# Kernel tuning notes

Hardware: AMD Instinct MI355X
Metric: run time of the kernel (lower is better)

The kernel has to match this reference:

```python
import jax, jax.numpy as jnp
import numpy as np

Z_DIM = 3
H = 128
N_BLOCKS = 4
N = 30000
E = 180000
T = 2


def _mlp2(x, W1, b1, W2, b2):
    return jnp.maximum(x @ W1 + b1, 0.0) @ W2 + b2


def _stats(x, eps=1e-8):
    # batch mean/std as accumulated by the running-stat Normalizer (buffers -> no grad)
    m = x.mean(0)
    v = jnp.maximum((x * x).mean(0) - m * m, 0.0)
    s = jnp.maximum(jnp.sqrt(v), eps)
    return jax.lax.stop_gradient(m), jax.lax.stop_gradient(s)


def setup_inputs() -> dict:
    key = jax.random.key(0)
    ks = jax.random.split(key, 32)

    def w(k, shape, fan_in):
        return jax.random.normal(k, shape, jnp.float32) / np.sqrt(fan_in).astype(np.float32)

    inp = {}
    inp["z"] = jax.random.normal(ks[0], (T, N, Z_DIM), jnp.float32)
    inp["z_target"] = jax.random.normal(ks[1], (N, Z_DIM), jnp.float32)
    inp["pos"] = jax.random.uniform(ks[2], (N, 2), jnp.float32)
    # encoder node MLP: z_dim -> H -> H
    inp["enc_node_W1"] = w(ks[3], (Z_DIM, H), Z_DIM)
    inp["enc_node_b1"] = jnp.zeros((H,), jnp.float32)
    inp["enc_node_W2"] = w(ks[4], (H, H), H)
    inp["enc_node_b2"] = jnp.zeros((H,), jnp.float32)
    # encoder edge MLP: edge_dim(3) -> H -> H
    inp["enc_edge_W1"] = w(ks[5], (3, H), 3)
    inp["enc_edge_b1"] = jnp.zeros((H,), jnp.float32)
    inp["enc_edge_W2"] = w(ks[6], (H, H), H)
    inp["enc_edge_b2"] = jnp.zeros((H,), jnp.float32)
    # decoder MLP: H -> H -> z_dim
    inp["dec_W1"] = w(ks[7], (H, H), H)
    inp["dec_b1"] = jnp.zeros((H,), jnp.float32)
    inp["dec_W2"] = w(ks[8], (H, Z_DIM), H)
    inp["dec_b2"] = jnp.zeros((Z_DIM,), jnp.float32)
    # GraphNetBlocks, stacked over n_blocks
    inp["blk_edge_W1"] = w(ks[9], (N_BLOCKS, 3 * H, H), 3 * H)
    inp["blk_edge_b1"] = jnp.zeros((N_BLOCKS, H), jnp.float32)
    inp["blk_edge_W2"] = w(ks[10], (N_BLOCKS, H, H), H)
    inp["blk_edge_b2"] = jnp.zeros((N_BLOCKS, H), jnp.float32)
    inp["blk_node_W1"] = w(ks[11], (N_BLOCKS, 2 * H, H), 2 * H)
    inp["blk_node_b1"] = jnp.zeros((N_BLOCKS, H), jnp.float32)
    inp["blk_node_W2"] = w(ks[12], (N_BLOCKS, H, H), H)
    inp["blk_node_b2"] = jnp.zeros((N_BLOCKS, H), jnp.float32)
    # bidirectional mesh edges (triangles_to_edges output)
    inp["senders"] = jax.random.randint(ks[13], (E,), 0, N, jnp.int64)
    inp["receivers"] = jax.random.randint(ks[14], (E,), 0, N, jnp.int64)
    return inp


def reference(z, z_target, pos,
              enc_node_W1, enc_node_b1, enc_node_W2, enc_node_b2,
              enc_edge_W1, enc_edge_b1, enc_edge_W2, enc_edge_b2,
              dec_W1, dec_b1, dec_W2, dec_b2,
              blk_edge_W1, blk_edge_b1, blk_edge_W2, blk_edge_b2,
              blk_node_W1, blk_node_b1, blk_node_W2, blk_node_b2,
              senders, receivers):
    zl = z[-1]                                   # [N, z_dim]
    n_nodes = zl.shape[0]

    # --- build_graph ---
    rel = pos[senders] - pos[receivers]          # [E, 2]
    ef_raw = jnp.concatenate([rel, jnp.linalg.norm(rel, axis=1, keepdims=True)], axis=1)  # [E, 3]
    em, es = _stats(ef_raw)
    ef = _mlp2((ef_raw - em) / es, enc_edge_W1, enc_edge_b1, enc_edge_W2, enc_edge_b2)    # [E, H]
    nm, ns = _stats(zl)
    nf = _mlp2((zl - nm) / ns, enc_node_W1, enc_node_b1, enc_node_W2, enc_node_b2)        # [N, H]

    # --- message passing blocks ---
    def block(carry, p):
        nf, ef = carry
        eW1, eb1, eW2, eb2, nW1, nb1, nW2, nb2 = p
        e_in = jnp.concatenate([ef, nf[senders], nf[receivers]], axis=1)   # [E, 3H]
        ef = _mlp2(e_in, eW1, eb1, eW2, eb2) + ef
        agg = jax.ops.segment_sum(ef, receivers, num_segments=n_nodes)    # [N, H]
        n_in = jnp.concatenate([nf, agg], axis=1)                          # [N, 2H]
        nf = _mlp2(n_in, nW1, nb1, nW2, nb2) + nf
        return (nf, ef), None

    (nf, ef), _ = jax.lax.scan(block, (nf, ef),
                               (blk_edge_W1, blk_edge_b1, blk_edge_W2, blk_edge_b2,
                                blk_node_W1, blk_node_b1, blk_node_W2, blk_node_b2))

    # --- decode + loss ---
    output = _mlp2(nf, dec_W1, dec_b1, dec_W2, dec_b2)                     # [N, z_dim]
    target = z_target - zl
    om, os = _stats(target)
    target_normalized = (target - om) / os
    loss = jnp.mean((target_normalized - output) ** 2)

    z_update = jax.lax.stop_gradient(output) * os + om                     # Normalizer.inverse(detach)
    z_pred = zl + z_update
    rmse = jnp.mean(jnp.sqrt(jnp.mean((z_pred - z_target) ** 2, axis=0)))
    return z_pred, loss, rmse
```

## Files before the change

kernel.cpp:

```cpp
#include <hip/hip_runtime.h>
#include <hip/hip_bf16.h>
#include <math.h>

#define HDIM 128
#define TPB 256

typedef __attribute__((ext_vector_type(8))) short bf16x8;
typedef __attribute__((ext_vector_type(4))) float f32x4;

static inline int ceil_div(int a, int b){ return (a + b - 1) / b; }

__device__ __forceinline__ float wave_sum(float v){
#pragma unroll
  for (int o = 32; o > 0; o >>= 1) v += __shfl_down(v, o, 64);
  return v;
}
__device__ __forceinline__ int wave_sum_i(int v){
#pragma unroll
  for (int o = 32; o > 0; o >>= 1) v += __shfl_down(v, o, 64);
  return v;
}

__device__ __forceinline__ short f2bf(float f){
  __hip_bfloat16 h = __float2bfloat16(f);
  return *reinterpret_cast<short*>(&h);
}
__device__ __forceinline__ float bfb2f(short s){
  unsigned int u = ((unsigned int)(unsigned short)s) << 16;
  return __builtin_bit_cast(float, u);
}

__device__ __forceinline__ void gl_lds16(const short* g, short* l){
  __builtin_amdgcn_global_load_lds(
      (const __attribute__((address_space(1))) void*)g,
      (__attribute__((address_space(3))) void*)l, 16, 0, 0);
}

__global__ void prep_a(const int* __restrict__ rcv, int* __restrict__ deg, int E, int neb,
                       const float* __restrict__ zl, const float* __restrict__ zt,
                       float* __restrict__ npart, int N, int nnb,
                       const float* __restrict__ encEW2,
                       const float* __restrict__ encNW2,
                       const float* __restrict__ decW1,
                       const float* __restrict__ beW1,
                       const float* __restrict__ beW2,
                       const float* __restrict__ bnW1,
                       const float* __restrict__ bnW2,
                       __hip_bfloat16* __restrict__ wp){
  __shared__ float red[4][12];
  const int bx = blockIdx.x, tid = threadIdx.x;
  if (bx < neb){
    int e = bx * 256 + tid;
    if (e < E) atomicAdd(&deg[rcv[e]], 1);
    return;
  }
  if (bx < neb + nnb){
    int b = bx - neb;
    int w = tid >> 6, l = tid & 63;
    int n = b * 256 + tid;
    float s[12];
#pragma unroll
    for (int i = 0; i < 12; i++) s[i] = 0.f;
    if (n < N){
#pragma unroll
      for (int d = 0; d < 3; d++){
        float z = zl[3*n+d];
        float t = zt[3*n+d] - z;
        s[d]   = z;  s[3+d] = z*z;
        s[6+d] = t;  s[9+d] = t*t;
      }
    }
#pragma unroll
    for (int i = 0; i < 12; i++) s[i] = wave_sum(s[i]);
    if (l == 0)
#pragma unroll
      for (int i = 0; i < 12; i++) red[w][i] = s[i];
    __syncthreads();
    if (tid < 12)
      npart[(size_t)b * 12 + tid] =
        red[0][tid] + red[1][tid] + red[2][tid] + red[3][tid];
    return;
  }
  int pid = bx - neb - nnb;
  int y = pid / 192;
  int x = pid - y * 192;
  const float* src; __hip_bfloat16* dst; int K;
  if (y == 0){ src = encEW2; dst = wp;          K = 128; }
  else if (y == 1){ src = encNW2; dst = wp + 16384; K = 128; }
  else if (y == 2){ src = decW1;  dst = wp + 32768; K = 128; }
  else {
    int b = (y - 3) >> 2, j = (y - 3) & 3;
    __hip_bfloat16* base = wp + 49152 + b * 114688;
    if (j == 0){ src = beW1 + b*49152; dst = base;          K = 384; }
    else if (j == 1){ src = beW2 + b*16384; dst = base + 49152; K = 128; }
    else if (j == 2){ src = bnW1 + b*32768; dst = base + 65536; K = 256; }
    else { src = bnW2 + b*16384; dst = base + 98304; K = 128; }
  }
  int id = x * 256 + tid;
  if (id >= 128 * K) return;
  int c = id >> 12;
  int r = id & 4095;
  int t = r >> 9;
  int l = (r >> 3) & 63;
  int j = r & 7;
  int k = c * 32 + ((l >> 4) << 3) + j;
  int n = t * 16 + (l & 15);
  dst[id] = __float2bfloat16(src[k * 128 + n]);
}

__global__ void scan_pass1(const int* __restrict__ deg, int* __restrict__ bsum, int N){
  __shared__ int red[4];
  int tid = threadIdx.x;
  int base = blockIdx.x * 1024;
  int s = 0;
  for (int i = tid; i < 1024; i += 256){
    int idx = base + i;
    if (idx < N) s += deg[idx];
  }
  s = wave_sum_i(s);
  if ((tid & 63) == 0) red[tid >> 6] = s;
  __syncthreads();
  if (tid == 0) bsum[blockIdx.x] = red[0] + red[1] + red[2] + red[3];
}

__global__ void scan_pass3(const int* __restrict__ deg, const int* __restrict__ bsum,
                           int nsb, int* __restrict__ cursor, int N){
  __shared__ int tsum[256];
  __shared__ int base_s;
  int tid = threadIdx.x;
  if (tid == 0){
    int acc = 0;
    for (int b = 0; b < (int)blockIdx.x; b++) acc += bsum[b];
    base_s = acc;
  }
  int base = blockIdx.x * 1024;
  int i0 = base + tid * 4;
  int v[4];
  int s = 0;
#pragma unroll
  for (int k = 0; k < 4; k++){
    int idx = i0 + k;
    v[k] = (idx < N) ? deg[idx] : 0;
    s += v[k];
  }
  tsum[tid] = s;
  __syncthreads();
  for (int off = 1; off < 256; off <<= 1){
    int val = (tid >= off) ? tsum[tid - off] : 0;
    __syncthreads();
    tsum[tid] += val;
    __syncthreads();
  }
  int excl = (tid == 0) ? 0 : tsum[tid - 1];
  int b = base_s + excl;
#pragma unroll
  for (int k = 0; k < 4; k++){
    int idx = i0 + k;
    if (idx < N){
      cursor[idx] = b;
      b += v[k];
    }
  }
}

__global__ void edge_prep(const float* __restrict__ pos,
                          const int* __restrict__ snd,
                          const int* __restrict__ rcv,
                          int* __restrict__ cursor,
                          int* __restrict__ psnd,
                          int* __restrict__ prcv,
                          float* __restrict__ ef_raw,
                          float* __restrict__ epart, int E){
  __shared__ float red[4][6];
  int tid = threadIdx.x, w = tid >> 6, l = tid & 63;
  int e = blockIdx.x * blockDim.x + tid;
  float s[6] = {0.f,0.f,0.f,0.f,0.f,0.f};
  if (e < E){
    int si = snd[e], ri = rcv[e];
    int p = atomicAdd(&cursor[ri], 1);
    psnd[p] = si;
    prcv[p] = ri;
    float rx = pos[2*si]   - pos[2*ri];
    float ry = pos[2*si+1] - pos[2*ri+1];
    float nm = sqrtf(rx*rx + ry*ry);
    ef_raw[3*p]   = rx;
    ef_raw[3*p+1] = ry;
    ef_raw[3*p+2] = nm;
    s[0] = rx; s[1] = ry; s[2] = nm;
    s[3] = rx*rx; s[4] = ry*ry; s[5] = nm*nm;
  }
#pragma unroll
  for (int k = 0; k < 6; k++) s[k] = wave_sum(s[k]);
  if (l == 0)
#pragma unroll
    for (int k = 0; k < 6; k++) red[w][k] = s[k];
  __syncthreads();
  if (tid < 6)
    epart[(size_t)blockIdx.x * 6 + tid] =
      red[0][tid] + red[1][tid] + red[2][tid] + red[3][tid];
}

__global__ void reduce_finalize(const float* __restrict__ ep, int ne,
                                const float* __restrict__ np_, int nn,
                                float* __restrict__ fin, int E, int N){
  __shared__ float red[4];
  __shared__ float raw[18];
  int tid = threadIdx.x, w = tid >> 6, l = tid & 63;
  for (int j = 0; j < 6; j++){
    float s = 0.f;
    for (int b = tid; b < ne; b += 256) s += ep[(size_t)b * 6 + j];
    s = wave_sum(s);
    if (l == 0) red[w] = s;
    __syncthreads();
    if (tid == 0) raw[j] = red[0] + red[1] + red[2] + red[3];
    __syncthreads();
  }
  for (int j = 0; j < 12; j++){
    float s = 0.f;
    for (int b = tid; b < nn; b += 256) s += np_[(size_t)b * 12 + j];
    s = wave_sum(s);
    if (l == 0) red[w] = s;
    __syncthreads();
    if (tid == 0) raw[6 + j] = red[0] + red[1] + red[2] + red[3];
    __syncthreads();
  }
  if (tid == 0){
#pragma unroll
    for (int d = 0; d < 3; d++){
      float cE = (float)E, cN = (float)N;
      float m, v;
      m = raw[0+d] / cE; v = fmaxf(raw[3+d]/cE - m*m, 0.f);
      fin[0+d] = m;  fin[3+d]  = fmaxf(sqrtf(v), 1e-8f);
      m = raw[6+d] / cN; v = fmaxf(raw[9+d]/cN - m*m, 0.f);
      fin[6+d] = m;  fin[9+d]  = fmaxf(sqrtf(v), 1e-8f);
      m = raw[12+d] / cN; v = fmaxf(raw[15+d]/cN - m*m, 0.f);
      fin[12+d] = m; fin[15+d] = fmaxf(sqrtf(v), 1e-8f);
    }
  }
}

__launch_bounds__(256)
__global__ void encoder_both(const float* __restrict__ eraw,
                             const float* __restrict__ zl,
                             const float* __restrict__ fin,
                             const float* __restrict__ eW1, const float* __restrict__ eb1,
                             const float* __restrict__ nW1, const float* __restrict__ nb1,
                             const __hip_bfloat16* __restrict__ wp,
                             const float* __restrict__ eb2, const float* __restrict__ nb2,
                             __hip_bfloat16* __restrict__ efo, __hip_bfloat16* __restrict__ nfo,
                             int E, int N, int EB){
  __shared__ __align__(16) short bsh[16384];
  const int tid = threadIdx.x, w = tid >> 6, l = tid & 63, m = l & 15, q = l >> 4;
  const bool ise = ((int)blockIdx.x < EB);
  const float* raw = ise ? eraw : zl;
  const float* mptr = fin + (ise ? 0 : 6);
  const float* sptr = fin + (ise ? 3 : 9);
  const float* W1 = ise ? eW1 : nW1;
  const float* b1 = ise ? eb1 : nb1;
  const float* b2 = ise ? eb2 : nb2;
  const short* wsrc = (const short*)wp + (ise ? 0 : 16384);
  __hip_bfloat16* out = ise ? efo : nfo;
  const int rows = ise ? E : N;
  const int bx = ise ? (int)blockIdx.x : (int)blockIdx.x - EB;
#pragma unroll
  for (int i = 0; i < 8; i++){
    int inst = w * 8 + i;
    gl_lds16(wsrc + inst * 512 + l * 8, &bsh[inst * 512]);
  }
  float s0 = mptr[0], s1 = mptr[1], s2 = mptr[2];
  float d0 = sptr[0], d1 = sptr[1], d2 = sptr[2];
  const int row0 = bx * 64 + w * 16;
  const int ra = min(row0 + m, rows - 1);
  float x0 = (raw[3*ra]   - s0) / d0;
  float x1 = (raw[3*ra+1] - s1) / d1;
  float x2 = (raw[3*ra+2] - s2) / d2;
  bf16x8 afr[4];
#pragma unroll
  for (int c = 0; c < 4; c++){
    int nb = c * 32 + q * 8;
#pragma unroll
    for (int j = 0; j < 8; j++){
      float h = b1[nb+j] + x0 * W1[nb+j] + x1 * W1[128+nb+j] + x2 * W1[256+nb+j];
      afr[c][j] = f2bf(fmaxf(h, 0.f));
    }
  }
  f32x4 acc[8];
#pragma unroll
  for (int t = 0; t < 8; t++) acc[t] = (f32x4){0.f,0.f,0.f,0.f};
  __syncthreads();
#pragma unroll
  for (int c = 0; c < 4; c++){
#pragma unroll
    for (int t = 0; t < 8; t++){
      bf16x8 b = *(const bf16x8*)&bsh[(c*8 + t)*512 + l*8];
      acc[t] = __builtin_amdgcn_mfma_f32_16x16x32_bf16(afr[c], b, acc[t], 0, 0, 0);
    }
  }
  const int row_d = row0 + q * 4;
#pragma unroll
  for (int t = 0; t < 8; t++){
    int col = t * 16 + m;
    float bb = b2[col];
#pragma unroll
    for (int r = 0; r < 4; r++){
      int e = row_d + r;
      if (e < rows) out[(size_t)e * HDIM + col] = __float2bfloat16(acc[t][r] + bb);
    }
  }
}

__launch_bounds__(256)
__global__ void msg_pre(const __hip_bfloat16* __restrict__ nf,
                        const __hip_bfloat16* __restrict__ eWf,
                        __hip_bfloat16* __restrict__ u,
                        float* __restrict__ agg, int N){
  __shared__ __align__(16) short wsh[16384];
  const int tid = threadIdx.x, w = tid >> 6, l = tid & 63, m = l & 15, q = l >> 4;
  const short* wsrc = (const short*)eWf + 4 * 4096;
#pragma unroll
  for (int i = 0; i < 8; i++){
    int f = w * 8 + i;
    gl_lds16(wsrc + f * 512 + l * 8, &wsh[f * 512]);
  }
  {
    float* az = agg + (size_t)blockIdx.x * 8192;
#pragma unroll
    for (int i = 0; i < 8; i++)
      *(f32x4*)(az + (size_t)(i * 256 + tid) * 4) = (f32x4){0.f,0.f,0.f,0.f};
  }
  const int row0 = blockIdx.x * 64 + w * 16;
  const int ra = min(row0 + m, N - 1);
  const short* pa = (const short*)nf + (size_t)ra * HDIM + q * 8;
  bf16x8 afr[4];
#pragma unroll
  for (int c = 0; c < 4; c++) afr[c] = *(const bf16x8*)(pa + c * 32);
  f32x4 acc[8];
#pragma unroll
  for (int t = 0; t < 8; t++) acc[t] = (f32x4){0.f,0.f,0.f,0.f};
  __syncthreads();
#pragma unroll
  for (int c = 0; c < 4; c++)
#pragma unroll
    for (int t = 0; t < 8; t++){
      bf16x8 b = *(const bf16x8*)&wsh[(c*8 + t)*512 + l*8];
      acc[t] = __builtin_amdgcn_mfma_f32_16x16x32_bf16(afr[c], b, acc[t], 0, 0, 0);
    }
  const int row_d = row0 + q * 4;
#pragma unroll
  for (int t = 0; t < 8; t++){
    int col = t * 16 + m;
#pragma unroll
    for (int r = 0; r < 4; r++){
      int n = row_d + r;
      if (n < N) u[(size_t)n * 256 + col] = __float2bfloat16(acc[t][r]);
    }
  }
  __syncthreads();
#pragma unroll
  for (int i = 0; i < 8; i++){
    int f = w * 8 + i;
    gl_lds16(wsrc + 16384 + f * 512 + l * 8, &wsh[f * 512]);
  }
#pragma unroll
  for (int t = 0; t < 8; t++) acc[t] = (f32x4){0.f,0.f,0.f,0.f};
  __syncthreads();
#pragma unroll
  for (int c = 0; c < 4; c++)
#pragma unroll
    for (int t = 0; t < 8; t++){
      bf16x8 b = *(const bf16x8*)&wsh[(c*8 + t)*512 + l*8];
      acc[t] = __builtin_amdgcn_mfma_f32_16x16x32_bf16(afr[c], b, acc[t], 0, 0, 0);
    }
#pragma unroll
  for (int t = 0; t < 8; t++){
    int col = 128 + t * 16 + m;
#pragma unroll
    for (int r = 0; r < 4; r++){
      int n = row_d + r;
      if (n < N) u[(size_t)n * 256 + col] = __float2bfloat16(acc[t][r]);
    }
  }
}

__launch_bounds__(512)
__global__ void edge_block(const int* __restrict__ psnd,
                           const int* __restrict__ prcv,
                           const __hip_bfloat16* __restrict__ u,
                           __hip_bfloat16* __restrict__ ef,
                           const __hip_bfloat16* __restrict__ Wfrag,
                           const float* __restrict__ b1,
                           const float* __restrict__ b2,
                           float* __restrict__ agg,
                           int do_write, int E){
  __shared__ __align__(16) short bsh[16384];
  __shared__ __align__(16) short hsh[8][16][136];
  __shared__ int rsh[128];
  const int tid = threadIdx.x, w = tid >> 6, l = tid & 63, m = l & 15, q = l >> 4;
  const short* wsrc = (const short*)Wfrag;
  const int row0 = blockIdx.x * 128 + w * 16;
  const int grow = min(row0 + (l >> 2), E - 1);
  const int us_row = psnd[grow], ur_row = prcv[grow];
  if ((l & 3) == 0) rsh[w * 16 + (l >> 2)] = ur_row;
#pragma unroll
  for (int i = 0; i < 4; i++){
    int inst = i * 8 + w;
    gl_lds16(wsrc + inst * 512 + l * 8, &bsh[inst * 512]);
  }
  const int ra = min(row0 + m, E - 1);
  const short* pe = (const short*)ef + (size_t)ra * HDIM + q * 8;
  bf16x8 afr[4];
#pragma unroll
  for (int c = 0; c < 4; c++) afr[c] = *(const bf16x8*)(pe + c * 32);
  {
    const short* pus = (const short*)u + (size_t)us_row * 256 + (l & 3) * 32;
    const short* pur = (const short*)u + (size_t)ur_row * 256 + 128 + (l & 3) * 32;
    short* hdst = &hsh[w][l >> 2][(l & 3) * 32];
#pragma unroll
    for (int k = 0; k < 4; k++){
      bf16x8 a = *(const bf16x8*)(pus + k * 8);
      bf16x8 b = *(const bf16x8*)(pur + k * 8);
      bf16x8 s;
#pragma unroll
      for (int j = 0; j < 8; j++) s[j] = f2bf(bfb2f(a[j]) + bfb2f(b[j]));
      *(bf16x8*)(hdst + k * 8) = s;
    }
  }
  f32x4 acc[8];
#pragma unroll
  for (int t = 0; t < 8; t++) acc[t] = (f32x4){0.f,0.f,0.f,0.f};
  __syncthreads();
#pragma unroll
  for (int c = 0; c < 4; c++){
#pragma unroll
    for (int t = 0; t < 8; t++){
      bf16x8 b = *(const bf16x8*)&bsh[(c*8 + t)*512 + l*8];
      acc[t] = __builtin_amdgcn_mfma_f32_16x16x32_bf16(afr[c], b, acc[t], 0, 0, 0);
    }
  }
  __syncthreads();
#pragma unroll
  for (int i = 0; i < 4; i++){
    int inst = i * 8 + w;
    gl_lds16(wsrc + 49152 + inst * 512 + l * 8, &bsh[inst * 512]);
  }
#pragma unroll
  for (int t = 0; t < 8; t++){
    float bb = b1[t * 16 + m];
#pragma unroll
    for (int r = 0; r < 4; r++){
      float uval = bfb2f(hsh[w][q*4 + r][t*16 + m]);
      hsh[w][q*4 + r][t*16 + m] = f2bf(fmaxf(acc[t][r] + uval + bb, 0.f));
    }
  }
  __syncthreads();
  bf16x8 ah[4];
  const short* ph = &hsh[w][m][0] + q * 8;
#pragma unroll
  for (int c = 0; c < 4; c++) ah[c] = *(const bf16x8*)(ph + c * 32);
#pragma unroll
  for (int t = 0; t < 8; t++) acc[t] = (f32x4){0.f,0.f,0.f,0.f};
#pragma unroll
  for (int c = 0; c < 4; c++){
#pragma unroll
    for (int t = 0; t < 8; t++){
      bf16x8 b = *(const bf16x8*)&bsh[(c*8 + t)*512 + l*8];
      acc[t] = __builtin_amdgcn_mfma_f32_16x16x32_bf16(ah[c], b, acc[t], 0, 0, 0);
    }
  }
#pragma unroll
  for (int t = 0; t < 8; t++){
    float bb = b2[t * 16 + m];
#pragma unroll
    for (int r = 0; r < 4; r++)
      hsh[w][q*4 + r][t*16 + m] = f2bf(acc[t][r] + bb);
  }
  const int orow = row0 + (l >> 2);
  const int orc = min(orow, E - 1);
  const short* pold = (const short*)ef + (size_t)orc * HDIM + (l & 3) * 32;
  short* hslot = &hsh[w][l >> 2][(l & 3) * 32];
  short* dst = (short*)ef + (size_t)orc * HDIM + (l & 3) * 32;
  const bool wr = (orow < E) && do_write;
#pragma unroll
  for (int k = 0; k < 4; k++){
    bf16x8 vnew = *(const bf16x8*)(hslot + k * 8);
    bf16x8 vo   = *(const bf16x8*)(pold + k * 8);
    bf16x8 vr;
#pragma unroll
    for (int j = 0; j < 8; j++) vr[j] = f2bf(bfb2f(vnew[j]) + bfb2f(vo[j]));
    *(bf16x8*)(hslot + k * 8) = vr;
    if (wr) *(bf16x8*)(dst + k * 8) = vr;
  }
  __syncthreads();
  {
    const int c = tid & 127;
    const int g = tid >> 7;
    const int nval = min(128, E - (int)blockIdx.x * 128);
    const int e0 = g * 32;
    if (e0 < nval){
      const int e1 = min(e0 + 32, nval);
      float run = 0.f; int cur = -1; int runstart = e0;
#pragma unroll
      for (int half = 0; half < 2; half++){
        float v[16]; int rv[16];
#pragma unroll
        for (int k = 0; k < 16; k++){
          int e = e0 + half * 16 + k;
          v[k]  = bfb2f(hsh[(e >> 4) & 7][e & 15][c]);
          rv[k] = rsh[e & 127];
        }
#pragma unroll
        for (int k = 0; k < 16; k++){
          int e = e0 + half * 16 + k;
          if (e < e1){
            if (rv[k] != cur){
              if (cur >= 0){
                if (runstart == e0) atomicAdd(&agg[(size_t)cur * 128 + c], run);
                else                agg[(size_t)cur * 128 + c] = run;
              }
              cur = rv[k]; run = 0.f; runstart = e;
            }
            run += v[k];
          }
        }
      }
      atomicAdd(&agg[(size_t)cur * 128 + c], run);
    }
  }
}

#define NB_COMPUTE_CHUNK(c) do {                                               \
  const short* bb_ = &bsh[(((c) >> 1) & 1) * 8192 + ((c) & 1) * 4096];         \
  _Pragma("unroll")                                                            \
  for (int t = 0; t < 8; t++){                                                 \
    bf16x8 b = *(const bf16x8*)(bb_ + t * 512 + l * 8);                        \
    acc[t] = __builtin_amdgcn_mfma_f32_16x16x32_bf16(afr[c], b, acc[t], 0, 0, 0); \
  }                                                                            \
} while(0)

__launch_bounds__(256)
__global__ void node_block(const float* __restrict__ agg,
                           __hip_bfloat16* __restrict__ nf,
                           const __hip_bfloat16* __restrict__ Wfrag,
                           const float* __restrict__ b1,
                           const float* __restrict__ b2,
                           int N){
  __shared__ __align__(16) short bsh[16384];
  __shared__ __align__(16) short hsh[4][16][136];
  const int tid = threadIdx.x, w = tid >> 6, l = tid & 63, m = l & 15, q = l >> 4;
  const short* wsrc = (const short*)Wfrag;
  auto stage_pair = [&](int p){
    const short* s = wsrc + p * 8192;
    short* d = &bsh[(p & 1) * 8192];
#pragma unroll
    for (int i = 0; i < 4; i++)
      gl_lds16(s + (i*4 + w)*512 + l*8, d + (i*4 + w)*512);
  };
  stage_pair(0); stage_pair(1);

  const int row0 = blockIdx.x * 64 + w * 16;
  const int ra = min(row0 + m, N - 1);
  const short* pn = (const short*)nf + (size_t)ra * HDIM + q * 8;
  bf16x8 afr[8];
#pragma unroll
  for (int c = 0; c < 4; c++) afr[c] = *(const bf16x8*)(pn + c * 32);

  const float* pag = agg + (size_t)ra * 128 + q * 8;
#pragma unroll
  for (int c = 0; c < 4; c++){
    f32x4 a0 = *(const f32x4*)(pag + c * 32);
    f32x4 a1 = *(const f32x4*)(pag + c * 32 + 4);
#pragma unroll
    for (int j = 0; j < 4; j++){
      afr[4 + c][j]     = f2bf(a0[j]);
      afr[4 + c][4 + j] = f2bf(a1[j]);
    }
  }

  f32x4 acc[8];
#pragma unroll
  for (int t = 0; t < 8; t++) acc[t] = (f32x4){0.f,0.f,0.f,0.f};
  __syncthreads();
  NB_COMPUTE_CHUNK(0);
  NB_COMPUTE_CHUNK(1);
  __syncthreads();
  stage_pair(2);
  NB_COMPUTE_CHUNK(2);
  NB_COMPUTE_CHUNK(3);
  __syncthreads();
  stage_pair(3);
  NB_COMPUTE_CHUNK(4);
  NB_COMPUTE_CHUNK(5);
  __syncthreads();
  NB_COMPUTE_CHUNK(6);
  NB_COMPUTE_CHUNK(7);
  __syncthreads();
  {
    const short* s = wsrc + 32768;
#pragma unroll
    for (int i = 0; i < 8; i++)
      gl_lds16(s + (i*4 + w)*512 + l*8, &bsh[(i*4 + w)*512]);
  }
#pragma unroll
  for (int t = 0; t < 8; t++){
    float bb = b1[t * 16 + m];
#pragma unroll
    for (int r = 0; r < 4; r++)
      hsh[w][q*4 + r][t*16 + m] = f2bf(fmaxf(acc[t][r] + bb, 0.f));
  }
  __syncthreads();
  const short* ph = &hsh[w][m][0] + q * 8;
#pragma unroll
  for (int t = 0; t < 8; t++) acc[t] = (f32x4){0.f,0.f,0.f,0.f};
#pragma unroll
  for (int c = 0; c < 4; c++){
    bf16x8 a = *(const bf16x8*)(ph + c * 32);
#pragma unroll
    for (int t = 0; t < 8; t++){
      bf16x8 b = *(const bf16x8*)&bsh[(c*8 + t)*512 + l*8];
      acc[t] = __builtin_amdgcn_mfma_f32_16x16x32_bf16(a, b, acc[t], 0, 0, 0);
    }
  }
#pragma unroll
  for (int t = 0; t < 8; t++){
    float bb = b2[t * 16 + m];
#pragma unroll
    for (int r = 0; r < 4; r++)
      hsh[w][q*4 + r][t*16 + m] = f2bf(acc[t][r] + bb);
  }
  const int orow = row0 + (l >> 2);
  if (orow < N){
    const short* pold = (const short*)nf + (size_t)orow * HDIM + (l & 3) * 32;
    const short* src = &hsh[w][l >> 2][(l & 3) * 32];
    short* dst = (short*)nf + (size_t)orow * HDIM + (l & 3) * 32;
#pragma unroll
    for (int k = 0; k < 4; k++){
      bf16x8 vnew = *(const bf16x8*)(src + k * 8);
      bf16x8 vo   = *(const bf16x8*)(pold + k * 8);
      bf16x8 vr;
#pragma unroll
      for (int j = 0; j < 8; j++) vr[j] = f2bf(bfb2f(vnew[j]) + bfb2f(vo[j]));
      *(bf16x8*)(dst + k * 8) = vr;
    }
  }
}

__launch_bounds__(256)
__global__ void dec_fused(const __hip_bfloat16* __restrict__ A,
                          const __hip_bfloat16* __restrict__ Wf,
                          const float* __restrict__ b1,
                          const float* __restrict__ W2,
                          const float* __restrict__ b2,
                          const float* __restrict__ zl,
                          const float* __restrict__ z_target,
                          const float* __restrict__ fin,
                          float* __restrict__ d_out,
                          float* __restrict__ lred,
                          unsigned int* __restrict__ cnt,
                          int N){
  __shared__ __align__(16) short bsh[16384];
  __shared__ float Wl[HDIM * 3];
  __shared__ float red[4][4];
  const int tid = threadIdx.x, w = tid >> 6, l = tid & 63, m = l & 15, q = l >> 4;
  const short* wsrc = (const short*)Wf;
#pragma unroll
  for (int i = 0; i < 8; i++){
    int inst = w * 8 + i;
    gl_lds16(wsrc + inst * 512 + l * 8, &bsh[inst * 512]);
  }
  for (int i = tid; i < HDIM * 3; i += 256) Wl[i] = W2[i];
  const int row0 = blockIdx.x * 64 + w * 16;
  const int ra = min(row0 + m, N - 1);
  const short* pa = (const short*)A + (size_t)ra * HDIM + q * 8;
  bf16x8 afr[4];
#pragma unroll
  for (int c = 0; c < 4; c++) afr[c] = *(const bf16x8*)(pa + c * 32);
  f32x4 acc[8];
#pragma unroll
  for (int t = 0; t < 8; t++) acc[t] = (f32x4){0.f,0.f,0.f,0.f};
  __syncthreads();
#pragma unroll
  for (int c = 0; c < 4; c++){
#pragma unroll
    for (int t = 0; t < 8; t++){
      bf16x8 b = *(const bf16x8*)&bsh[(c*8 + t)*512 + l*8];
      acc[t] = __builtin_amdgcn_mfma_f32_16x16x32_bf16(afr[c], b, acc[t], 0, 0, 0);
    }
  }
  float p0[4] = {0,0,0,0}, p1[4] = {0,0,0,0}, p2[4] = {0,0,0,0};
#pragma unroll
  for (int t = 0; t < 8; t++){
    int col = t * 16 + m;
    float bb = b1[col];
    float w0 = Wl[col*3], w1 = Wl[col*3+1], w2 = Wl[col*3+2];
#pragma unroll
    for (int r = 0; r < 4; r++){
      float h = fmaxf(acc[t][r] + bb, 0.f);
      p0[r] += h * w0; p1[r] += h * w1; p2[r] += h * w2;
    }
  }
#pragma unroll
  for (int r = 0; r < 4; r++){
#pragma unroll
    for (int o = 1; o < 16; o <<= 1){
      p0[r] += __shfl_xor(p0[r], o, 64);
      p1[r] += __shfl_xor(p1[r], o, 64);
      p2[r] += __shfl_xor(p2[r], o, 64);
    }
  }
  float s[4] = {0.f,0.f,0.f,0.f};
  if (m == 0){
#pragma unroll
    for (int r = 0; r < 4; r++){
      int n = row0 + q * 4 + r;
      if (n < N){
        float pd[3] = {p0[r], p1[r], p2[r]};
#pragma unroll
        for (int d = 0; d < 3; d++){
          float o   = pd[d] + b2[d];
          float om = fin[12 + d], os = fin[15 + d];
          float zld = zl[3*n + d];
          float zt  = z_target[3*n + d];
          float tn  = ((zt - zld) - om) / os;
          float diff = tn - o;
          s[0] += diff * diff;
          float zp = zld + o * os + om;
          d_out[3*n + d] = zp;
          float e = zp - zt;
          s[1 + d] += e * e;
        }
      }
    }
  }
#pragma unroll
  for (int k = 0; k < 4; k++) s[k] = wave_sum(s[k]);
  if (l == 0)
#pragma unroll
    for (int k = 0; k < 4; k++) red[w][k] = s[k];
  __syncthreads();
  if (tid < 4)
    atomicAdd(&lred[tid], red[0][tid] + red[1][tid] + red[2][tid] + red[3][tid]);
  __syncthreads();
  if (tid == 0){
    __threadfence();
    unsigned int t = atomicAdd(cnt, 1u);
    if (t == gridDim.x - 1){
      float vals[4];
#pragma unroll
      for (int k = 0; k < 4; k++) vals[k] = atomicAdd(&lred[k], 0.f);
      float cN = (float)N;
      float loss = vals[0] / (3.f * cN);
      float rmse = (sqrtf(vals[1]/cN) + sqrtf(vals[2]/cN) + sqrtf(vals[3]/cN)) / 3.f;
      d_out[(size_t)3 * N]     = loss;
      d_out[(size_t)3 * N + 1] = rmse;
    }
  }
}

extern "C" void kernel_launch(void* const* d_in, const int* in_sizes, int n_in,
                              void* d_out, int out_size, void* d_ws, size_t ws_size,
                              hipStream_t stream){
  const float* z           = (const float*)d_in[0];
  const float* z_target    = (const float*)d_in[1];
  const float* pos         = (const float*)d_in[2];
  const float* enc_node_W1 = (const float*)d_in[3];
  const float* enc_node_b1 = (const float*)d_in[4];
  const float* enc_node_W2 = (const float*)d_in[5];
  const float* enc_node_b2 = (const float*)d_in[6];
  const float* enc_edge_W1 = (const float*)d_in[7];
  const float* enc_edge_b1 = (const float*)d_in[8];
  const float* enc_edge_W2 = (const float*)d_in[9];
  const float* enc_edge_b2 = (const float*)d_in[10];
  const float* dec_W1      = (const float*)d_in[11];
  const float* dec_b1      = (const float*)d_in[12];
  const float* dec_W2      = (const float*)d_in[13];
  const float* dec_b2      = (const float*)d_in[14];
  const float* blk_edge_W1 = (const float*)d_in[15];
  const float* blk_edge_b1 = (const float*)d_in[16];
  const float* blk_edge_W2 = (const float*)d_in[17];
  const float* blk_edge_b2 = (const float*)d_in[18];
  const float* blk_node_W1 = (const float*)d_in[19];
  const float* blk_node_b1 = (const float*)d_in[20];
  const float* blk_node_W2 = (const float*)d_in[21];
  const float* blk_node_b2 = (const float*)d_in[22];
  const int*   senders     = (const int*)d_in[23];
  const int*   receivers   = (const int*)d_in[24];

  const int N = in_sizes[1] / 3;
  const int E = in_sizes[23];
  const float* zl = z + (size_t)N * 3;

  const int neb = ceil_div(E, TPB);
  const int nnb = ceil_div(N, TPB);
  const int nsb = ceil_div(N, 1024);
  const int EB  = ceil_div(E, 64);
  const int NB  = ceil_div(N, 64);

  char* p = (char*)d_ws;
  auto carve = [&](size_t bytes) -> char* {
    char* r = p; p += (bytes + 255) & ~(size_t)255; return r;
  };
  float* stats_fin = (float*)carve(32 * 4);
  float* epart     = (float*)carve((size_t)neb * 6 * 4);
  float* npart     = (float*)carve((size_t)nnb * 12 * 4);
  float* ef_raw    = (float*)carve((size_t)E * 3 * 4);
  int*   deg       = (int*)carve((size_t)(N + 16) * 4);
  float* lred      = (float*)(deg + N);
  unsigned int* cnt = (unsigned int*)(deg + N + 4);
  int*   bsum      = (int*)carve((size_t)(nsb + 1) * 4);
  int*   cursor    = (int*)carve((size_t)N * 4);
  int*   psnd      = (int*)carve((size_t)E * 4);
  int*   prcv      = (int*)carve((size_t)E * 4);
  float* agg       = (float*)carve(((size_t)N + 64) * 128 * 4);
  __hip_bfloat16* wp = (__hip_bfloat16*)carve((size_t)507904 * 2);
  __hip_bfloat16* ef = (__hip_bfloat16*)carve((size_t)E * HDIM * 2);
  __hip_bfloat16* nf = (__hip_bfloat16*)carve((size_t)N * HDIM * 2);
  __hip_bfloat16* u  = (__hip_bfloat16*)carve((size_t)N * 256 * 2);

  float* out = (float*)d_out;

  hipMemsetAsync(deg, 0, (size_t)(N + 16) * 4, stream);

  prep_a<<<neb + nnb + 3648, TPB, 0, stream>>>(receivers, deg, E, neb,
                                               zl, z_target, npart, N, nnb,
                                               enc_edge_W2, enc_node_W2, dec_W1,
                                               blk_edge_W1, blk_edge_W2,
                                               blk_node_W1, blk_node_W2, wp);
  scan_pass1<<<nsb, TPB, 0, stream>>>(deg, bsum, N);
  scan_pass3<<<nsb, TPB, 0, stream>>>(deg, bsum, nsb, cursor, N);
  edge_prep<<<neb, TPB, 0, stream>>>(pos, senders, receivers, cursor,
                                     psnd, prcv, ef_raw, epart, E);
  reduce_finalize<<<1, TPB, 0, stream>>>(epart, neb, npart, nnb, stats_fin, E, N);

  encoder_both<<<EB + NB, TPB, 0, stream>>>(ef_raw, zl, stats_fin,
                                            enc_edge_W1, enc_edge_b1,
                                            enc_node_W1, enc_node_b1,
                                            wp, enc_edge_b2, enc_node_b2,
                                            ef, nf, E, N, EB);

  for (int b = 0; b < 4; b++){
    const __hip_bfloat16* eWf = wp + 49152 + (size_t)b * 114688;
    const __hip_bfloat16* nWf = eWf + 65536;
    const float* eb1 = blk_edge_b1 + (size_t)b * 128;
    const float* eb2 = blk_edge_b2 + (size_t)b * 128;
    const float* nb1 = blk_node_b1 + (size_t)b * 128;
    const float* nb2 = blk_node_b2 + (size_t)b * 128;

    msg_pre<<<NB, TPB, 0, stream>>>(nf, eWf, u, agg, N);
    edge_block<<<ceil_div(E, 128), 512, 0, stream>>>(psnd, prcv, u, ef,
                                                     eWf, eb1, eb2, agg,
                                                     (b < 3) ? 1 : 0, E);
    node_block<<<NB, TPB, 0, stream>>>(agg, nf, nWf, nb1, nb2, N);
  }

  dec_fused<<<NB, TPB, 0, stream>>>(nf, wp + 32768, dec_b1, dec_W2, dec_b2,
                                    zl, z_target, stats_fin,
                                    out, lred, cnt, N);
}
```

Measured before the change: 488.9 us.

## Fuse sender/receiver projection into edge kernel and drop msg_pre precompute

Removes the per-node msg_pre kernel that precomputed sender and receiver projections into a u buffer. edge_block now gathers raw node features for sender and receiver and runs the full 3H-wide first-layer GEMM per edge, staging weight pairs into double-buffered LDS between syncs. Zeroing of agg moves to a one-time memset plus clearing inside node_block after the read. This saves one launch per block and the u buffer writes and reads, but roughly triples the first-layer MFMA work, since it now runs over edges instead of nodes.

Result: no change. 491.2 us (+0.5%).

```diff
diff --git a/kernel.cpp b/kernel.cpp
--- a/kernel.cpp
+++ b/kernel.cpp
@@ -309,83 +309,19 @@
   }
 }
 
-__launch_bounds__(256)
-__global__ void msg_pre(const __hip_bfloat16* __restrict__ nf,
-                        const __hip_bfloat16* __restrict__ eWf,
-                        __hip_bfloat16* __restrict__ u,
-                        float* __restrict__ agg, int N){
-  __shared__ __align__(16) short wsh[16384];
-  const int tid = threadIdx.x, w = tid >> 6, l = tid & 63, m = l & 15, q = l >> 4;
-  const short* wsrc = (const short*)eWf + 4 * 4096;
-#pragma unroll
-  for (int i = 0; i < 8; i++){
-    int f = w * 8 + i;
-    gl_lds16(wsrc + f * 512 + l * 8, &wsh[f * 512]);
-  }
-  {
-    float* az = agg + (size_t)blockIdx.x * 8192;
-#pragma unroll
-    for (int i = 0; i < 8; i++)
-      *(f32x4*)(az + (size_t)(i * 256 + tid) * 4) = (f32x4){0.f,0.f,0.f,0.f};
-  }
-  const int row0 = blockIdx.x * 64 + w * 16;
-  const int ra = min(row0 + m, N - 1);
-  const short* pa = (const short*)nf + (size_t)ra * HDIM + q * 8;
-  bf16x8 afr[4];
-#pragma unroll
-  for (int c = 0; c < 4; c++) afr[c] = *(const bf16x8*)(pa + c * 32);
-  f32x4 acc[8];
-#pragma unroll
-  for (int t = 0; t < 8; t++) acc[t] = (f32x4){0.f,0.f,0.f,0.f};
-  __syncthreads();
-#pragma unroll
-  for (int c = 0; c < 4; c++)
-#pragma unroll
-    for (int t = 0; t < 8; t++){
-      bf16x8 b = *(const bf16x8*)&wsh[(c*8 + t)*512 + l*8];
-      acc[t] = __builtin_amdgcn_mfma_f32_16x16x32_bf16(afr[c], b, acc[t], 0, 0, 0);
-    }
-  const int row_d = row0 + q * 4;
-#pragma unroll
-  for (int t = 0; t < 8; t++){
-    int col = t * 16 + m;
-#pragma unroll
-    for (int r = 0; r < 4; r++){
-      int n = row_d + r;
-      if (n < N) u[(size_t)n * 256 + col] = __float2bfloat16(acc[t][r]);
-    }
-  }
-  __syncthreads();
-#pragma unroll
-  for (int i = 0; i < 8; i++){
-    int f = w * 8 + i;
-    gl_lds16(wsrc + 16384 + f * 512 + l * 8, &wsh[f * 512]);
-  }
-#pragma unroll
-  for (int t = 0; t < 8; t++) acc[t] = (f32x4){0.f,0.f,0.f,0.f};
-  __syncthreads();
-#pragma unroll
-  for (int c = 0; c < 4; c++)
-#pragma unroll
-    for (int t = 0; t < 8; t++){
-      bf16x8 b = *(const bf16x8*)&wsh[(c*8 + t)*512 + l*8];
-      acc[t] = __builtin_amdgcn_mfma_f32_16x16x32_bf16(afr[c], b, acc[t], 0, 0, 0);
-    }
-#pragma unroll
-  for (int t = 0; t < 8; t++){
-    int col = 128 + t * 16 + m;
-#pragma unroll
-    for (int r = 0; r < 4; r++){
-      int n = row_d + r;
-      if (n < N) u[(size_t)n * 256 + col] = __float2bfloat16(acc[t][r]);
-    }
-  }
-}
+#define EB_CHUNK(cidx, afrag) do {                                             \
+  const short* bb_ = &bsh[(((cidx) >> 1) & 1) * 8192 + ((cidx) & 1) * 4096];   \
+  _Pragma("unroll")                                                            \
+  for (int t = 0; t < 8; t++){                                                 \
+    bf16x8 b = *(const bf16x8*)(bb_ + t * 512 + l * 8);                        \
+    acc[t] = __builtin_amdgcn_mfma_f32_16x16x32_bf16(afrag, b, acc[t], 0, 0, 0); \
+  }                                                                            \
+} while(0)
 
 __launch_bounds__(512)
 __global__ void edge_block(const int* __restrict__ psnd,
                            const int* __restrict__ prcv,
-                           const __hip_bfloat16* __restrict__ u,
+                           const __hip_bfloat16* __restrict__ nf,
                            __hip_bfloat16* __restrict__ ef,
                            const __hip_bfloat16* __restrict__ Wfrag,
                            const float* __restrict__ b1,
@@ -398,59 +334,60 @@
   const int tid = threadIdx.x, w = tid >> 6, l = tid & 63, m = l & 15, q = l >> 4;
   const short* wsrc = (const short*)Wfrag;
   const int row0 = blockIdx.x * 128 + w * 16;
-  const int grow = min(row0 + (l >> 2), E - 1);
-  const int us_row = psnd[grow], ur_row = prcv[grow];
-  if ((l & 3) == 0) rsh[w * 16 + (l >> 2)] = ur_row;
-#pragma unroll
-  for (int i = 0; i < 4; i++){
-    int inst = i * 8 + w;
-    gl_lds16(wsrc + inst * 512 + l * 8, &bsh[inst * 512]);
-  }
   const int ra = min(row0 + m, E - 1);
+  const int rs = psnd[ra], rr = prcv[ra];
+  if (q == 0) rsh[w * 16 + m] = rr;
+  auto stage_pair = [&](int p){
+    const short* s = wsrc + p * 8192;
+    short* d = &bsh[(p & 1) * 8192];
+    gl_lds16(s + (w*2)  *512 + l*8, d + (w*2)  *512);
+    gl_lds16(s + (w*2+1)*512 + l*8, d + (w*2+1)*512);
+  };
+  auto stage_w2 = [&](int j){
+    const short* s = wsrc + 49152 + j * 8192;
+    short* d = &bsh[j * 8192];
+    gl_lds16(s + (w*2)  *512 + l*8, d + (w*2)  *512);
+    gl_lds16(s + (w*2+1)*512 + l*8, d + (w*2+1)*512);
+  };
+  stage_pair(0); stage_pair(1);
   const short* pe = (const short*)ef + (size_t)ra * HDIM + q * 8;
-  bf16x8 afr[4];
-#pragma unroll
-  for (int c = 0; c < 4; c++) afr[c] = *(const bf16x8*)(pe + c * 32);
-  {
-    const short* pus = (const short*)u + (size_t)us_row * 256 + (l & 3) * 32;
-    const short* pur = (const short*)u + (size_t)ur_row * 256 + 128 + (l & 3) * 32;
-    short* hdst = &hsh[w][l >> 2][(l & 3) * 32];
-#pragma unroll
-    for (int k = 0; k < 4; k++){
-      bf16x8 a = *(const bf16x8*)(pus + k * 8);
-      bf16x8 b = *(const bf16x8*)(pur + k * 8);
-      bf16x8 s;
-#pragma unroll
-      for (int j = 0; j < 8; j++) s[j] = f2bf(bfb2f(a[j]) + bfb2f(b[j]));
-      *(bf16x8*)(hdst + k * 8) = s;
-    }
+  const short* ps = (const short*)nf + (size_t)rs * HDIM + q * 8;
+  const short* pr = (const short*)nf + (size_t)rr * HDIM + q * 8;
+  bf16x8 afr_e[4], afr_s[4], afr_r[4];
+#pragma unroll
+  for (int c = 0; c < 4; c++){
+    afr_e[c] = *(const bf16x8*)(pe + c * 32);
+    afr_s[c] = *(const bf16x8*)(ps + c * 32);
+    afr_r[c] = *(const bf16x8*)(pr + c * 32);
   }
   f32x4 acc[8];
 #pragma unroll
   for (int t = 0; t < 8; t++) acc[t] = (f32x4){0.f,0.f,0.f,0.f};
   __syncthreads();
-#pragma unroll
-  for (int c = 0; c < 4; c++){
-#pragma unroll
-    for (int t = 0; t < 8; t++){
-      bf16x8 b = *(const bf16x8*)&bsh[(c*8 + t)*512 + l*8];
-      acc[t] = __builtin_amdgcn_mfma_f32_16x16x32_bf16(afr[c], b, acc[t], 0, 0, 0);
-    }
-  }
-  __syncthreads();
-#pragma unroll
-  for (int i = 0; i < 4; i++){
-    int inst = i * 8 + w;
-    gl_lds16(wsrc + 49152 + inst * 512 + l * 8, &bsh[inst * 512]);
-  }
+  EB_CHUNK(0, afr_e[0]); EB_CHUNK(1, afr_e[1]);
+  __syncthreads();
+  stage_pair(2);
+  EB_CHUNK(2, afr_e[2]); EB_CHUNK(3, afr_e[3]);
+  __syncthreads();
+  stage_pair(3);
+  EB_CHUNK(4, afr_s[0]); EB_CHUNK(5, afr_s[1]);
+  __syncthreads();
+  stage_pair(4);
+  EB_CHUNK(6, afr_s[2]); EB_CHUNK(7, afr_s[3]);
+  __syncthreads();
+  stage_pair(5);
+  EB_CHUNK(8, afr_r[0]); EB_CHUNK(9, afr_r[1]);
+  __syncthreads();
+  stage_w2(0);
+  EB_CHUNK(10, afr_r[2]); EB_CHUNK(11, afr_r[3]);
+  __syncthreads();
+  stage_w2(1);
 #pragma unroll
   for (int t = 0; t < 8; t++){
     float bb = b1[t * 16 + m];
 #pragma unroll
-    for (int r = 0; r < 4; r++){
-      float uval = bfb2f(hsh[w][q*4 + r][t*16 + m]);
-      hsh[w][q*4 + r][t*16 + m] = f2bf(fmaxf(acc[t][r] + uval + bb, 0.f));
-    }
+    for (int r = 0; r < 4; r++)
+      hsh[w][q*4 + r][t*16 + m] = f2bf(fmaxf(acc[t][r] + bb, 0.f));
   }
   __syncthreads();
   bf16x8 ah[4];
@@ -459,14 +396,7 @@
   for (int c = 0; c < 4; c++) ah[c] = *(const bf16x8*)(ph + c * 32);
 #pragma unroll
   for (int t = 0; t < 8; t++) acc[t] = (f32x4){0.f,0.f,0.f,0.f};
-#pragma unroll
-  for (int c = 0; c < 4; c++){
-#pragma unroll
-    for (int t = 0; t < 8; t++){
-      bf16x8 b = *(const bf16x8*)&bsh[(c*8 + t)*512 + l*8];
-      acc[t] = __builtin_amdgcn_mfma_f32_16x16x32_bf16(ah[c], b, acc[t], 0, 0, 0);
-    }
-  }
+  EB_CHUNK(0, ah[0]); EB_CHUNK(1, ah[1]); EB_CHUNK(2, ah[2]); EB_CHUNK(3, ah[3]);
 #pragma unroll
   for (int t = 0; t < 8; t++){
     float bb = b2[t * 16 + m];
@@ -538,12 +468,12 @@
 } while(0)
 
 __launch_bounds__(256)
-__global__ void node_block(const float* __restrict__ agg,
+__global__ void node_block(float* __restrict__ agg,
                            __hip_bfloat16* __restrict__ nf,
                            const __hip_bfloat16* __restrict__ Wfrag,
                            const float* __restrict__ b1,
                            const float* __restrict__ b2,
-                           int N){
+                           int do_zero, int N){
   __shared__ __align__(16) short bsh[16384];
   __shared__ __align__(16) short hsh[4][16][136];
   const int tid = threadIdx.x, w = tid >> 6, l = tid & 63, m = l & 15, q = l >> 4;
@@ -564,7 +494,7 @@
 #pragma unroll
   for (int c = 0; c < 4; c++) afr[c] = *(const bf16x8*)(pn + c * 32);
 
-  const float* pag = agg + (size_t)ra * 128 + q * 8;
+  float* pag = agg + (size_t)ra * 128 + q * 8;
 #pragma unroll
   for (int c = 0; c < 4; c++){
     f32x4 a0 = *(const f32x4*)(pag + c * 32);
@@ -573,6 +503,13 @@
     for (int j = 0; j < 4; j++){
       afr[4 + c][j]     = f2bf(a0[j]);
       afr[4 + c][4 + j] = f2bf(a1[j]);
+    }
+  }
+  if (do_zero && (row0 + m) < N){
+#pragma unroll
+    for (int c = 0; c < 4; c++){
+      *(f32x4*)(pag + c * 32)     = (f32x4){0.f,0.f,0.f,0.f};
+      *(f32x4*)(pag + c * 32 + 4) = (f32x4){0.f,0.f,0.f,0.f};
     }
   }
 
@@ -814,11 +751,11 @@
   __hip_bfloat16* wp = (__hip_bfloat16*)carve((size_t)507904 * 2);
   __hip_bfloat16* ef = (__hip_bfloat16*)carve((size_t)E * HDIM * 2);
   __hip_bfloat16* nf = (__hip_bfloat16*)carve((size_t)N * HDIM * 2);
-  __hip_bfloat16* u  = (__hip_bfloat16*)carve((size_t)N * 256 * 2);
 
   float* out = (float*)d_out;
 
   hipMemsetAsync(deg, 0, (size_t)(N + 16) * 4, stream);
+  hipMemsetAsync(agg, 0, ((size_t)N + 64) * 128 * 4, stream);
 
   prep_a<<<neb + nnb + 3648, TPB, 0, stream>>>(receivers, deg, E, neb,
                                                zl, z_target, npart, N, nnb,
@@ -845,11 +782,11 @@
     const float* nb1 = blk_node_b1 + (size_t)b * 128;
     const float* nb2 = blk_node_b2 + (size_t)b * 128;
 
-    msg_pre<<<NB, TPB, 0, stream>>>(nf, eWf, u, agg, N);
-    edge_block<<<ceil_div(E, 128), 512, 0, stream>>>(psnd, prcv, u, ef,
+    edge_block<<<ceil_div(E, 128), 512, 0, stream>>>(psnd, prcv, nf, ef,
                                                      eWf, eb1, eb2, agg,
                                                      (b < 3) ? 1 : 0, E);
-    node_block<<<NB, TPB, 0, stream>>>(agg, nf, nWf, nb1, nb2, N);
+    node_block<<<NB, TPB, 0, stream>>>(agg, nf, nWf, nb1, nb2,
+                                       (b < 3) ? 1 : 0, N);
   }
 
   dec_fused<<<NB, TPB, 0, stream>>>(nf, wp + 32768, dec_b1, dec_W2, dec_b2,
```

## Read MFMA weight fragments directly from global memory instead of staging in LDS

Applied to the files above, without the earlier changes.

In the encoder, msg_pre, node_block and decoder kernels, the weight fragments are no longer copied into shared memory. Each lane now loads its bf16x8 B operand straight from the global (L2-cached) fragment array. This removes the LDS staging, several barriers and the double-buffered pipelining in node_block, and it lowers LDS use, which may allow more blocks per CU. In exchange, every wave issues its own global loads for the weights, so each MFMA now depends on global/L2 latency instead of LDS latency.

New measurement: 505.2 us. +3.3%, slower.

```diff
diff --git a/kernel.cpp b/kernel.cpp
--- a/kernel.cpp
+++ b/kernel.cpp
@@ -249,7 +249,6 @@
                              const float* __restrict__ eb2, const float* __restrict__ nb2,
                              __hip_bfloat16* __restrict__ efo, __hip_bfloat16* __restrict__ nfo,
                              int E, int N, int EB){
-  __shared__ __align__(16) short bsh[16384];
   const int tid = threadIdx.x, w = tid >> 6, l = tid & 63, m = l & 15, q = l >> 4;
   const bool ise = ((int)blockIdx.x < EB);
   const float* raw = ise ? eraw : zl;
@@ -262,11 +261,6 @@
   __hip_bfloat16* out = ise ? efo : nfo;
   const int rows = ise ? E : N;
   const int bx = ise ? (int)blockIdx.x : (int)blockIdx.x - EB;
-#pragma unroll
-  for (int i = 0; i < 8; i++){
-    int inst = w * 8 + i;
-    gl_lds16(wsrc + inst * 512 + l * 8, &bsh[inst * 512]);
-  }
   float s0 = mptr[0], s1 = mptr[1], s2 = mptr[2];
   float d0 = sptr[0], d1 = sptr[1], d2 = sptr[2];
   const int row0 = bx * 64 + w * 16;
@@ -287,12 +281,11 @@
   f32x4 acc[8];
 #pragma unroll
   for (int t = 0; t < 8; t++) acc[t] = (f32x4){0.f,0.f,0.f,0.f};
-  __syncthreads();
 #pragma unroll
   for (int c = 0; c < 4; c++){
 #pragma unroll
     for (int t = 0; t < 8; t++){
-      bf16x8 b = *(const bf16x8*)&bsh[(c*8 + t)*512 + l*8];
+      bf16x8 b = *(const bf16x8*)(wsrc + (c*8 + t)*512 + l*8);
       acc[t] = __builtin_amdgcn_mfma_f32_16x16x32_bf16(afr[c], b, acc[t], 0, 0, 0);
     }
   }
@@ -314,14 +307,9 @@
                         const __hip_bfloat16* __restrict__ eWf,
                         __hip_bfloat16* __restrict__ u,
                         float* __restrict__ agg, int N){
-  __shared__ __align__(16) short wsh[16384];
   const int tid = threadIdx.x, w = tid >> 6, l = tid & 63, m = l & 15, q = l >> 4;
-  const short* wsrc = (const short*)eWf + 4 * 4096;
-#pragma unroll
-  for (int i = 0; i < 8; i++){
-    int f = w * 8 + i;
-    gl_lds16(wsrc + f * 512 + l * 8, &wsh[f * 512]);
-  }
+  const short* ws = (const short*)eWf + 4 * 4096;
+  const short* wr_ = (const short*)eWf + 8 * 4096;
   {
     float* az = agg + (size_t)blockIdx.x * 8192;
 #pragma unroll
@@ -337,12 +325,11 @@
   f32x4 acc[8];
 #pragma unroll
   for (int t = 0; t < 8; t++) acc[t] = (f32x4){0.f,0.f,0.f,0.f};
-  __syncthreads();
 #pragma unroll
   for (int c = 0; c < 4; c++)
 #pragma unroll
     for (int t = 0; t < 8; t++){
-      bf16x8 b = *(const bf16x8*)&wsh[(c*8 + t)*512 + l*8];
+      bf16x8 b = *(const bf16x8*)(ws + (c*8 + t)*512 + l*8);
       acc[t] = __builtin_amdgcn_mfma_f32_16x16x32_bf16(afr[c], b, acc[t], 0, 0, 0);
     }
   const int row_d = row0 + q * 4;
@@ -355,20 +342,13 @@
       if (n < N) u[(size_t)n * 256 + col] = __float2bfloat16(acc[t][r]);
     }
   }
-  __syncthreads();
-#pragma unroll
-  for (int i = 0; i < 8; i++){
-    int f = w * 8 + i;
-    gl_lds16(wsrc + 16384 + f * 512 + l * 8, &wsh[f * 512]);
-  }
 #pragma unroll
   for (int t = 0; t < 8; t++) acc[t] = (f32x4){0.f,0.f,0.f,0.f};
-  __syncthreads();
 #pragma unroll
   for (int c = 0; c < 4; c++)
 #pragma unroll
     for (int t = 0; t < 8; t++){
-      bf16x8 b = *(const bf16x8*)&wsh[(c*8 + t)*512 + l*8];
+      bf16x8 b = *(const bf16x8*)(wr_ + (c*8 + t)*512 + l*8);
       acc[t] = __builtin_amdgcn_mfma_f32_16x16x32_bf16(afr[c], b, acc[t], 0, 0, 0);
     }
 #pragma unroll
@@ -528,15 +508,6 @@
   }
 }
 
-#define NB_COMPUTE_CHUNK(c) do {                                               \
-  const short* bb_ = &bsh[(((c) >> 1) & 1) * 8192 + ((c) & 1) * 4096];         \
-  _Pragma("unroll")                                                            \
-  for (int t = 0; t < 8; t++){                                                 \
-    bf16x8 b = *(const bf16x8*)(bb_ + t * 512 + l * 8);                        \
-    acc[t] = __builtin_amdgcn_mfma_f32_16x16x32_bf16(afr[c], b, acc[t], 0, 0, 0); \
-  }                                                                            \
-} while(0)
-
 __launch_bounds__(256)
 __global__ void node_block(const float* __restrict__ agg,
                            __hip_bfloat16* __restrict__ nf,
@@ -544,18 +515,10 @@
                            const float* __restrict__ b1,
                            const float* __restrict__ b2,
                            int N){
-  __shared__ __align__(16) short bsh[16384];
   __shared__ __align__(16) short hsh[4][16][136];
   const int tid = threadIdx.x, w = tid >> 6, l = tid & 63, m = l & 15, q = l >> 4;
-  const short* wsrc = (const short*)Wfrag;
-  auto stage_pair = [&](int p){
-    const short* s = wsrc + p * 8192;
-    short* d = &bsh[(p & 1) * 8192];
-#pragma unroll
-    for (int i = 0; i < 4; i++)
-      gl_lds16(s + (i*4 + w)*512 + l*8, d + (i*4 + w)*512);
-  };
-  stage_pair(0); stage_pair(1);
+  const short* wg = (const short*)Wfrag;
+  const short* w2 = wg + 32768;
 
   const int row0 = blockIdx.x * 64 + w * 16;
   const int ra = min(row0 + m, N - 1);
@@ -579,26 +542,13 @@
   f32x4 acc[8];
 #pragma unroll
   for (int t = 0; t < 8; t++) acc[t] = (f32x4){0.f,0.f,0.f,0.f};
-  __syncthreads();
-  NB_COMPUTE_CHUNK(0);
-  NB_COMPUTE_CHUNK(1);
-  __syncthreads();
-  stage_pair(2);
-  NB_COMPUTE_CHUNK(2);
-  NB_COMPUTE_CHUNK(3);
-  __syncthreads();
-  stage_pair(3);
-  NB_COMPUTE_CHUNK(4);
-  NB_COMPUTE_CHUNK(5);
-  __syncthreads();
-  NB_COMPUTE_CHUNK(6);
-  NB_COMPUTE_CHUNK(7);
-  __syncthreads();
-  {
-    const short* s = wsrc + 32768;
-#pragma unroll
-    for (int i = 0; i < 8; i++)
-      gl_lds16(s + (i*4 + w)*512 + l*8, &bsh[(i*4 + w)*512]);
+#pragma unroll
+  for (int c = 0; c < 8; c++){
+#pragma unroll
+    for (int t = 0; t < 8; t++){
+      bf16x8 b = *(const bf16x8*)(wg + (c*8 + t)*512 + l*8);
+      acc[t] = __builtin_amdgcn_mfma_f32_16x16x32_bf16(afr[c], b, acc[t], 0, 0, 0);
+    }
   }
 #pragma unroll
   for (int t = 0; t < 8; t++){
@@ -616,10 +566,11 @@
     bf16x8 a = *(const bf16x8*)(ph + c * 32);
 #pragma unroll
     for (int t = 0; t < 8; t++){
-      bf16x8 b = *(const bf16x8*)&bsh[(c*8 + t)*512 + l*8];
+      bf16x8 b = *(const bf16x8*)(w2 + (c*8 + t)*512 + l*8);
       acc[t] = __builtin_amdgcn_mfma_f32_16x16x32_bf16(a, b, acc[t], 0, 0, 0);
     }
   }
+  __syncthreads();
 #pragma unroll
   for (int t = 0; t < 8; t++){
     float bb = b2[t * 16 + m];
@@ -657,17 +608,9 @@
                           float* __restrict__ lred,
                           unsigned int* __restrict__ cnt,
                           int N){
-  __shared__ __align__(16) short bsh[16384];
-  __shared__ float Wl[HDIM * 3];
   __shared__ float red[4][4];
   const int tid = threadIdx.x, w = tid >> 6, l = tid & 63, m = l & 15, q = l >> 4;
-  const short* wsrc = (const short*)Wf;
-#pragma unroll
-  for (int i = 0; i < 8; i++){
-    int inst = w * 8 + i;
-    gl_lds16(wsrc + inst * 512 + l * 8, &bsh[inst * 512]);
-  }
-  for (int i = tid; i < HDIM * 3; i += 256) Wl[i] = W2[i];
+  const short* wg = (const short*)Wf;
   const int row0 = blockIdx.x * 64 + w * 16;
   const int ra = min(row0 + m, N - 1);
   const short* pa = (const short*)A + (size_t)ra * HDIM + q * 8;
@@ -677,12 +620,11 @@
   f32x4 acc[8];
 #pragma unroll
   for (int t = 0; t < 8; t++) acc[t] = (f32x4){0.f,0.f,0.f,0.f};
-  __syncthreads();
 #pragma unroll
   for (int c = 0; c < 4; c++){
 #pragma unroll
     for (int t = 0; t < 8; t++){
-      bf16x8 b = *(const bf16x8*)&bsh[(c*8 + t)*512 + l*8];
+      bf16x8 b = *(const bf16x8*)(wg + (c*8 + t)*512 + l*8);
       acc[t] = __builtin_amdgcn_mfma_f32_16x16x32_bf16(afr[c], b, acc[t], 0, 0, 0);
     }
   }
@@ -691,11 +633,11 @@
   for (int t = 0; t < 8; t++){
     int col = t * 16 + m;
     float bb = b1[col];
-    float w0 = Wl[col*3], w1 = Wl[col*3+1], w2 = Wl[col*3+2];
+    float w0 = W2[col*3], w1 = W2[col*3+1], w2v = W2[col*3+2];
 #pragma unroll
     for (int r = 0; r < 4; r++){
       float h = fmaxf(acc[t][r] + bb, 0.f);
-      p0[r] += h * w0; p1[r] += h * w1; p2[r] += h * w2;
+      p0[r] += h * w0; p1[r] += h * w1; p2[r] += h * w2v;
     }
   }
 #pragma unroll
```
